# Optimization experiments

Hardware: AMD Instinct MI355X
Metric: run time of the kernel (lower is better)

## Reference

```python
import jax, jax.numpy as jnp
import numpy as np

NUM_HEADS = 4
DIM_MODEL = 256
DIM_HEAD = DIM_MODEL // NUM_HEADS  # 64


def _conv1x1(w, b, x):
    # Conv1d kernel_size=1: [B, D_in, N] -> [B, D_out, N]
    return jnp.einsum('oi,bin->bon', w, x) + b[None, :, None]


def setup_inputs() -> dict:
    key = jax.random.key(0)
    ks = jax.random.split(key, 12)
    B, D, N = 8, DIM_MODEL, 2048
    s = 1.0 / np.sqrt(D)
    inp = {
        'query': jax.random.normal(ks[0], (B, D, N), dtype=jnp.float32),
        'key': jax.random.normal(ks[1], (B, D, N), dtype=jnp.float32),
        'value': jax.random.normal(ks[2], (B, D, N), dtype=jnp.float32),
        'wq': jax.random.normal(ks[3], (D, D), dtype=jnp.float32) * s,
        'bq': jax.random.normal(ks[4], (D,), dtype=jnp.float32) * 0.01,
        'wk': jax.random.normal(ks[5], (D, D), dtype=jnp.float32) * s,
        'bk': jax.random.normal(ks[6], (D,), dtype=jnp.float32) * 0.01,
        'wv': jax.random.normal(ks[7], (D, D), dtype=jnp.float32) * s,
        'bv': jax.random.normal(ks[8], (D,), dtype=jnp.float32) * 0.01,
        'wm': jax.random.normal(ks[9], (D, D), dtype=jnp.float32) * s,
        'bm': jax.random.normal(ks[10], (D,), dtype=jnp.float32) * 0.01,
    }
    return inp


def reference(query, key, value, wq, bq, wk, bk, wv, bv, wm, bm):
    B = query.shape[0]
    d, h = DIM_HEAD, NUM_HEADS
    # 1x1 conv projections, then split channels as (dim_head, num_heads) per torch view
    q = _conv1x1(wq, bq, query).reshape(B, d, h, -1)  # [B, d, h, N]
    k = _conv1x1(wk, bk, key).reshape(B, d, h, -1)    # [B, d, h, M]
    v = _conv1x1(wv, bv, value).reshape(B, d, h, -1)  # [B, d, h, M]
    norm = 1.0 / float(d) ** 0.5
    scores = jnp.einsum('bdhn,bdhm->bhnm', q, k) * norm  # [B, h, N, M]
    prob = jax.nn.softmax(scores, axis=-1)
    attn = jnp.einsum('bhnm,bdhm->bdhn', prob, v)        # [B, d, h, N]
    out = _conv1x1(wm, bm, attn.reshape(B, d * h, -1))   # [B, D, N]
    return out
```

## Files before the change

kernel.cpp:

```cpp
#include <hip/hip_runtime.h>
#include <math.h>

#define BB 8
#define DD 256
#define NN 2048
#define NH 4
#define DH 64

typedef _Float16 half8   __attribute__((ext_vector_type(8)));
typedef _Float16 half4_t __attribute__((ext_vector_type(4)));
typedef float    floatx4 __attribute__((ext_vector_type(4)));

#define MFMA32(A, B, C) __builtin_amdgcn_mfma_f32_16x16x32_f16(A, B, C, 0, 0, 0)
#define MFMA16(A, B, C) __builtin_amdgcn_mfma_f32_16x16x16f16(A, B, C, 0, 0, 0)

#define SC 0.18033688011112042f

__global__ __launch_bounds__(256) void prep_weights(
    const float* __restrict__ wq, const float* __restrict__ wk,
    const float* __restrict__ wv, const float* __restrict__ wm,
    _Float16* __restrict__ wqf, _Float16* __restrict__ wkf,
    _Float16* __restrict__ wvf, _Float16* __restrict__ wmf)
{
    int id = blockIdx.x * 256 + threadIdx.x;
    wqf[id] = (_Float16)wq[id];
    wkf[id] = (_Float16)wk[id];
    wvf[id] = (_Float16)wv[id];
    int row = id >> 8, col = id & 255;
    int hh = col >> 6, dd = col & 63;
    wmf[id] = (_Float16)wm[row * 256 + dd * 4 + hh];
}


#define CONV_KLOOP(Wf)                                                        \
    half8 af[2][4][2];                                                        \
    {                                                                         \
        const _Float16* wp = (Wf) + (size_t)(w * 64 + c) * 256;               \
        _Pragma("unroll")                                                     \
        for (int rt = 0; rt < 4; ++rt)                                        \
            _Pragma("unroll")                                                 \
            for (int ch = 0; ch < 2; ++ch)                                    \
                af[0][rt][ch] =                                               \
                    *(const half8*)(wp + rt * 16 * 256 + ch * 32 + q * 8);    \
    }                                                                         \
    floatx4 acc[4][2];                                                        \
    _Pragma("unroll")                                                         \
    for (int rt = 0; rt < 4; ++rt)                                            \
        _Pragma("unroll")                                                     \
        for (int nt = 0; nt < 2; ++nt)                                        \
            acc[rt][nt] = (floatx4){0.f, 0.f, 0.f, 0.f};                      \
    _Pragma("unroll")                                                         \
    for (int kc = 0; kc < 4; ++kc) {                                          \
        const int cur = kc & 1;                                               \
        if (kc < 3) {                                                         \
            const _Float16* wp = (Wf) + (size_t)(w * 64 + c) * 256 +          \
                                 (kc + 1) * 64;                               \
            _Pragma("unroll")                                                 \
            for (int rt = 0; rt < 4; ++rt)                                    \
                _Pragma("unroll")                                             \
                for (int ch = 0; ch < 2; ++ch)                                \
                    af[cur ^ 1][rt][ch] = *(const half8*)(wp +                \
                        rt * 16 * 256 + ch * 32 + q * 8);                     \
        }                                                                     \
        half8 bx[2][2];                                                       \
        _Pragma("unroll")                                                     \
        for (int nt = 0; nt < 2; ++nt)                                        \
            _Pragma("unroll")                                                 \
            for (int ch = 0; ch < 2; ++ch)                                    \
                bx[nt][ch] = *(const half8*)(smem + (nt * 16 + c) * 264 +     \
                                             kc * 64 + ch * 32 + q * 8);      \
        _Pragma("unroll")                                                     \
        for (int nt = 0; nt < 2; ++nt)                                        \
            _Pragma("unroll")                                                 \
            for (int ch = 0; ch < 2; ++ch)                                    \
                _Pragma("unroll")                                             \
                for (int rt = 0; rt < 4; ++rt)                                \
                    acc[rt][nt] = MFMA32(af[cur][rt][ch], bx[nt][ch],         \
                                         acc[rt][nt]);                        \
    }

#define CONV_STAGE_F32(X)                                                     \
    {                                                                         \
        const int nb = t & 7, kb = t >> 3;                                    \
        const float* Xg = (X) + (size_t)b * DD * NN + (size_t)(kb * 8) * NN + \
                          n0 + nb * 4;                                        \
        float4 x[8];                                                          \
        _Pragma("unroll")                                                     \
        for (int i = 0; i < 8; ++i) x[i] = *(const float4*)(Xg + (size_t)i * NN); \
        _Pragma("unroll")                                                     \
        for (int j = 0; j < 4; ++j) {                                         \
            half8 hv;                                                         \
            _Pragma("unroll")                                                 \
            for (int i = 0; i < 8; ++i)                                       \
                hv[i] = (_Float16)(((const float*)&x[i])[j]);                 \
            *(half8*)(smem + (nb * 4 + j) * 264 + kb * 8) = hv;               \
        }                                                                     \
    }                                                                         \
    __syncthreads();

__global__ __launch_bounds__(256, 3) void conv_qk(
    const _Float16* __restrict__ wqf, const _Float16* __restrict__ wkf,
    const float* __restrict__ bq, const float* __restrict__ bk,
    const float* __restrict__ Xq, const float* __restrict__ Xk,
    _Float16* __restrict__ Yq, _Float16* __restrict__ Yk)
{
    const int n0 = blockIdx.x * 32;
    const int b  = blockIdx.y;
    const int pr = blockIdx.z;
    const _Float16* Wf = pr ? wkf : wqf;
    const float* bias  = pr ? bk : bq;
    const float* X     = pr ? Xk : Xq;
    _Float16* Y        = pr ? Yk : Yq;
    const float osc    = pr ? 1.0f : SC;

    const int t = threadIdx.x;
    const int w = t >> 6, l = t & 63, c = l & 15, q = l >> 4;

    __shared__ _Float16 smem[10240];

    CONV_STAGE_F32(X)
    CONV_KLOOP(Wf)

    __syncthreads();
    #pragma unroll
    for (int rt = 0; rt < 4; ++rt)
        #pragma unroll
        for (int nt = 0; nt < 2; ++nt) {
            half4_t hv;
            #pragma unroll
            for (int r = 0; r < 4; ++r)
                hv[r] = (_Float16)((acc[rt][nt][r] +
                        bias[w * 64 + rt * 16 + q * 4 + r]) * osc);
            *(half4_t*)(smem + (nt * 16 + c) * 264 + w * 64 + rt * 16 + q * 4) = hv;
        }
    __syncthreads();
    {
        const int rh = t >> 1, nn = rh >> 2, hh = rh & 3, off = (t & 1) * 32;
        const _Float16* src = smem + nn * 264 + hh;
        half8 hv[4];
        #pragma unroll
        for (int i = 0; i < 4; ++i)
            #pragma unroll
            for (int k = 0; k < 8; ++k)
                hv[i][k] = src[(off + i * 8 + k) * 4];
        _Float16* dst = Y + ((size_t)(b * NH + hh) * NN + n0 + nn) * 64 + off;
        #pragma unroll
        for (int i = 0; i < 4; ++i) *(half8*)(dst + i * 8) = hv[i];
    }
}

__global__ __launch_bounds__(256, 3) void conv_v(
    const _Float16* __restrict__ Wf, const float* __restrict__ bias,
    const float* __restrict__ X, _Float16* __restrict__ Y)
{
    const int n0 = blockIdx.x * 32;
    const int b  = blockIdx.y;
    const int t  = threadIdx.x;
    const int w  = t >> 6, l = t & 63, c = l & 15, q = l >> 4;

    __shared__ _Float16 smem[10240];

    CONV_STAGE_F32(X)
    CONV_KLOOP(Wf)

    __syncthreads();
    #pragma unroll
    for (int rt = 0; rt < 4; ++rt)
        #pragma unroll
        for (int nt = 0; nt < 2; ++nt)
            #pragma unroll
            for (int r = 0; r < 4; ++r)
                smem[(w * 64 + rt * 16 + q * 4 + r) * 40 + nt * 16 + c] =
                    (_Float16)(acc[rt][nt][r] + bias[w * 64 + rt * 16 + q * 4 + r]);
    __syncthreads();
    {
        const int dd = t >> 2, hh = t & 3;
        _Float16* dst = Y + ((size_t)(b * NH + hh) * 64 + dd) * NN + n0;
        #pragma unroll
        for (int i = 0; i < 4; ++i)
            *(half8*)(dst + i * 8) = *(const half8*)(smem + t * 40 + i * 8);
    }
}

__global__ __launch_bounds__(256, 3) void conv_o(
    const _Float16* __restrict__ Wf, const float* __restrict__ bias,
    const _Float16* __restrict__ At, float* __restrict__ out)
{
    const int n0 = blockIdx.x * 32;
    const int b  = blockIdx.y;
    const int t  = threadIdx.x;
    const int w  = t >> 6, l = t & 63, c = l & 15, q = l >> 4;

    __shared__ _Float16 smem[10240];

    {
        const int row = t >> 3, seg = (t & 7) * 32;
        const _Float16* Xg = At + ((size_t)b * NN + n0 + row) * 256 + seg;
        #pragma unroll
        for (int i = 0; i < 4; ++i)
            *(half8*)(smem + row * 264 + seg + i * 8) = *(const half8*)(Xg + i * 8);
    }
    __syncthreads();

    CONV_KLOOP(Wf)

    float* fs = (float*)smem;
    #pragma unroll
    for (int p = 0; p < 2; ++p) {
        __syncthreads();
        #pragma unroll
        for (int rtl = 0; rtl < 2; ++rtl) {
            const int rt = 2 * p + rtl;
            #pragma unroll
            for (int nt = 0; nt < 2; ++nt)
                #pragma unroll
                for (int r = 0; r < 4; ++r)
                    fs[(w * 32 + rtl * 16 + q * 4 + r) * 36 + nt * 16 + c] =
                        acc[rt][nt][r] + bias[w * 64 + rt * 16 + q * 4 + r];
        }
        __syncthreads();
        const int L = t >> 1, nloc = (t & 1) * 16;
        const int ww = L >> 5, rtl2 = (L >> 4) & 1, qq = (L >> 2) & 3, rr = L & 3;
        const int cout = ww * 64 + (2 * p + rtl2) * 16 + qq * 4 + rr;
        float* dst = out + (size_t)b * DD * NN + (size_t)cout * NN + n0 + nloc;
        #pragma unroll
        for (int i = 0; i < 4; ++i)
            *(float4*)(dst + 4 * i) = *(const float4*)(fs + L * 36 + nloc + 4 * i);
    }
}

__global__ __launch_bounds__(512) void attn_mfma4(
    const _Float16* __restrict__ Qt, const _Float16* __restrict__ Kt,
    const _Float16* __restrict__ V, _Float16* __restrict__ At)
{
    const int n0 = blockIdx.x * 128;
    const int h  = blockIdx.y;
    const int b  = blockIdx.z;
    const int t  = threadIdx.x;
    const int w  = t >> 6, l = t & 63, c = l & 15, q = l >> 4;

    const size_t bh = (size_t)(b * NH + h);

    __shared__ _Float16 smem[9216 + 8704];
    _Float16* Ks = smem;
    _Float16* Vs = smem + 9216;

    half8 bq2[2];
    #pragma unroll
    for (int ch = 0; ch < 2; ++ch)
        bq2[ch] = *(const half8*)(Qt + (bh * NN + n0 + w * 16 + c) * 64 + ch * 32 + q * 8);

    float lp = 0.f;
    floatx4 o[4];
    #pragma unroll
    for (int dt = 0; dt < 4; ++dt) o[dt] = (floatx4){0.f, 0.f, 0.f, 0.f};

    const int ksr = t >> 2, ksc = (t & 3) * 16;
    const int vr  = t >> 3, vcb = (t & 7) * 16;
    const _Float16* Kg = Kt + bh * NN * 64;
    const _Float16* Vg = V + bh * 64 * NN;

    for (int m0 = 0; m0 < NN; m0 += 128) {
        __syncthreads();
        *(half8*)(Ks + ksr * 72 + ksc) =
            *(const half8*)(Kg + (size_t)(m0 + ksr) * 64 + ksc);
        *(half8*)(Ks + ksr * 72 + ksc + 8) =
            *(const half8*)(Kg + (size_t)(m0 + ksr) * 64 + ksc + 8);
        #pragma unroll
        for (int u = 0; u < 2; ++u) {
            const int mb = vcb + u * 8;
            half8 v8 = *(const half8*)(Vg + (size_t)vr * NN + m0 + mb);
            const int p0 = (mb & ~31) + (((mb >> 2) & 3) << 3) + (((mb >> 4) & 1) << 2);
            half4_t lo, hi;
            #pragma unroll
            for (int j = 0; j < 4; ++j) { lo[j] = v8[j]; hi[j] = v8[4 + j]; }
            *(half4_t*)(Vs + vr * 136 + p0)     = lo;
            *(half4_t*)(Vs + vr * 136 + p0 + 8) = hi;
        }
        __syncthreads();

        #pragma unroll
        for (int mt2 = 0; mt2 < 4; ++mt2) {
            half4_t p[2];
            #pragma unroll
            for (int hf = 0; hf < 2; ++hf) {
                const int mt = mt2 * 2 + hf;
                floatx4 s = {0.f, 0.f, 0.f, 0.f};
                #pragma unroll
                for (int ch = 0; ch < 2; ++ch) {
                    half8 ak = *(const half8*)(Ks + (mt * 16 + c) * 72 + ch * 32 + q * 8);
                    s = MFMA32(ak, bq2[ch], s);
                }
                #pragma unroll
                for (int r = 0; r < 4; ++r) {
                    float e = exp2f(s[r]);
                    lp += e;
                    p[hf][r] = (_Float16)e;
                }
            }
            #pragma unroll
            for (int dt = 0; dt < 4; ++dt) {
                half8 av = *(const half8*)(Vs + (dt * 16 + c) * 136 + mt2 * 32 + q * 8);
                half4_t alo, ahi;
                #pragma unroll
                for (int j = 0; j < 4; ++j) { alo[j] = av[j]; ahi[j] = av[4 + j]; }
                o[dt] = MFMA16(alo, p[0], o[dt]);
                o[dt] = MFMA16(ahi, p[1], o[dt]);
            }
        }
    }

    lp += __shfl_xor(lp, 16);
    lp += __shfl_xor(lp, 32);
    const float inv = 1.f / lp;

    __syncthreads();
    #pragma unroll
    for (int dt = 0; dt < 4; ++dt) {
        half4_t ov;
        #pragma unroll
        for (int r = 0; r < 4; ++r) ov[r] = (_Float16)(o[dt][r] * inv);
        *(half4_t*)(smem + (w * 16 + c) * 72 + dt * 16 + q * 4) = ov;
    }
    __syncthreads();

    const int rn = t >> 2, roff = (t & 3) * 16;
    _Float16* dst = At + ((size_t)b * NN + n0 + rn) * 256 + h * 64 + roff;
    *(half8*)dst       = *(const half8*)(smem + rn * 72 + roff);
    *(half8*)(dst + 8) = *(const half8*)(smem + rn * 72 + roff + 8);
}

extern "C" void kernel_launch(void* const* d_in, const int* in_sizes, int n_in,
                              void* d_out, int out_size, void* d_ws, size_t ws_size,
                              hipStream_t stream) {
    const float* query = (const float*)d_in[0];
    const float* key_  = (const float*)d_in[1];
    const float* value = (const float*)d_in[2];
    const float* wq    = (const float*)d_in[3];
    const float* bq    = (const float*)d_in[4];
    const float* wk    = (const float*)d_in[5];
    const float* bk    = (const float*)d_in[6];
    const float* wv    = (const float*)d_in[7];
    const float* bv    = (const float*)d_in[8];
    const float* wm    = (const float*)d_in[9];
    const float* bm    = (const float*)d_in[10];
    float* out = (float*)d_out;

    _Float16* ws = (_Float16*)d_ws;
    _Float16* wqf = ws;
    _Float16* wkf = wqf + 65536;
    _Float16* wvf = wkf + 65536;
    _Float16* wmf = wvf + 65536;
    const size_t e16 = (size_t)BB * NH * NN * DH;
    _Float16* qf = ws + 262144;
    _Float16* kf = qf + e16;
    _Float16* vf = kf + e16;
    _Float16* at = vf + e16;

    prep_weights<<<256, 256, 0, stream>>>(wq, wk, wv, wm, wqf, wkf, wvf, wmf);
    conv_qk<<<dim3(64, 8, 2), 256, 0, stream>>>(wqf, wkf, bq, bk, query, key_, qf, kf);
    conv_v <<<dim3(64, 8, 1), 256, 0, stream>>>(wvf, bv, value, vf);
    attn_mfma4<<<dim3(16, 4, 8), 512, 0, stream>>>(qf, kf, vf, at);
    conv_o <<<dim3(64, 8, 1), 256, 0, stream>>>(wmf, bm, at, out);
}
```

Baseline: 218.0 us.

## Fuse Q/K/V projections into one launch, widen conv blocks, prefetch K/V in attention

Merges the separate Q/K and V projection kernels into a single conv_qkv launch with a z-dimension of three. The projection and output conv kernels move to 512-thread blocks that split the N tile across waves, each wave holding one accumulator column. The attention kernel gains register prefetching of the next K/V tile so the global loads overlap the MFMA work, and it uses packed cvt_pkrtz for the fp16 conversion of the exponentials. The aim is to cut launch overhead, shorten per-thread work and hide global-load latency, at the cost of more registers per thread in attention and round-toward-zero conversion instead of round-to-nearest.

```diff
diff --git a/kernel.cpp b/kernel.cpp
--- a/kernel.cpp
+++ b/kernel.cpp
@@ -9,6 +9,7 @@
 
 typedef _Float16 half8   __attribute__((ext_vector_type(8)));
 typedef _Float16 half4_t __attribute__((ext_vector_type(4)));
+typedef _Float16 half2_t __attribute__((ext_vector_type(2)));
 typedef float    floatx4 __attribute__((ext_vector_type(4)));
 
 #define MFMA32(A, B, C) __builtin_amdgcn_mfma_f32_16x16x32_f16(A, B, C, 0, 0, 0)
@@ -35,7 +36,7 @@
 #define CONV_KLOOP(Wf)                                                        \
     half8 af[2][4][2];                                                        \
     {                                                                         \
-        const _Float16* wp = (Wf) + (size_t)(w * 64 + c) * 256;               \
+        const _Float16* wp = (Wf) + (size_t)((w & 3) * 64 + c) * 256;         \
         _Pragma("unroll")                                                     \
         for (int rt = 0; rt < 4; ++rt)                                        \
             _Pragma("unroll")                                                 \
@@ -43,17 +44,14 @@
                 af[0][rt][ch] =                                               \
                     *(const half8*)(wp + rt * 16 * 256 + ch * 32 + q * 8);    \
     }                                                                         \
-    floatx4 acc[4][2];                                                        \
+    floatx4 acc[4];                                                           \
     _Pragma("unroll")                                                         \
-    for (int rt = 0; rt < 4; ++rt)                                            \
-        _Pragma("unroll")                                                     \
-        for (int nt = 0; nt < 2; ++nt)                                        \
-            acc[rt][nt] = (floatx4){0.f, 0.f, 0.f, 0.f};                      \
+    for (int rt = 0; rt < 4; ++rt) acc[rt] = (floatx4){0.f, 0.f, 0.f, 0.f};   \
     _Pragma("unroll")                                                         \
     for (int kc = 0; kc < 4; ++kc) {                                          \
         const int cur = kc & 1;                                               \
         if (kc < 3) {                                                         \
-            const _Float16* wp = (Wf) + (size_t)(w * 64 + c) * 256 +          \
+            const _Float16* wp = (Wf) + (size_t)((w & 3) * 64 + c) * 256 +    \
                                  (kc + 1) * 64;                               \
             _Pragma("unroll")                                                 \
             for (int rt = 0; rt < 4; ++rt)                                    \
@@ -62,127 +60,108 @@
                     af[cur ^ 1][rt][ch] = *(const half8*)(wp +                \
                         rt * 16 * 256 + ch * 32 + q * 8);                     \
         }                                                                     \
-        half8 bx[2][2];                                                       \
         _Pragma("unroll")                                                     \
-        for (int nt = 0; nt < 2; ++nt)                                        \
+        for (int ch = 0; ch < 2; ++ch) {                                      \
+            half8 bx = *(const half8*)(smem + ((w >> 2) * 16 + c) * 264 +     \
+                                       kc * 64 + ch * 32 + q * 8);            \
             _Pragma("unroll")                                                 \
-            for (int ch = 0; ch < 2; ++ch)                                    \
-                bx[nt][ch] = *(const half8*)(smem + (nt * 16 + c) * 264 +     \
-                                             kc * 64 + ch * 32 + q * 8);      \
-        _Pragma("unroll")                                                     \
-        for (int nt = 0; nt < 2; ++nt)                                        \
-            _Pragma("unroll")                                                 \
-            for (int ch = 0; ch < 2; ++ch)                                    \
-                _Pragma("unroll")                                             \
-                for (int rt = 0; rt < 4; ++rt)                                \
-                    acc[rt][nt] = MFMA32(af[cur][rt][ch], bx[nt][ch],         \
-                                         acc[rt][nt]);                        \
+            for (int rt = 0; rt < 4; ++rt)                                    \
+                acc[rt] = MFMA32(af[cur][rt][ch], bx, acc[rt]);               \
+        }                                                                     \
     }
 
 #define CONV_STAGE_F32(X)                                                     \
     {                                                                         \
         const int nb = t & 7, kb = t >> 3;                                    \
-        const float* Xg = (X) + (size_t)b * DD * NN + (size_t)(kb * 8) * NN + \
+        const float* Xg = (X) + (size_t)b * DD * NN + (size_t)(kb * 4) * NN + \
                           n0 + nb * 4;                                        \
-        float4 x[8];                                                          \
+        float4 x[4];                                                          \
         _Pragma("unroll")                                                     \
-        for (int i = 0; i < 8; ++i) x[i] = *(const float4*)(Xg + (size_t)i * NN); \
+        for (int i = 0; i < 4; ++i) x[i] = *(const float4*)(Xg + (size_t)i * NN); \
         _Pragma("unroll")                                                     \
         for (int j = 0; j < 4; ++j) {                                         \
-            half8 hv;                                                         \
+            half4_t hv;                                                       \
             _Pragma("unroll")                                                 \
-            for (int i = 0; i < 8; ++i)                                       \
+            for (int i = 0; i < 4; ++i)                                       \
                 hv[i] = (_Float16)(((const float*)&x[i])[j]);                 \
-            *(half8*)(smem + (nb * 4 + j) * 264 + kb * 8) = hv;               \
+            *(half4_t*)(smem + (nb * 4 + j) * 264 + kb * 4) = hv;             \
         }                                                                     \
     }                                                                         \
     __syncthreads();
 
-__global__ __launch_bounds__(256, 3) void conv_qk(
+__global__ __launch_bounds__(512, 4) void conv_qkv(
     const _Float16* __restrict__ wqf, const _Float16* __restrict__ wkf,
+    const _Float16* __restrict__ wvf,
     const float* __restrict__ bq, const float* __restrict__ bk,
+    const float* __restrict__ bv,
     const float* __restrict__ Xq, const float* __restrict__ Xk,
-    _Float16* __restrict__ Yq, _Float16* __restrict__ Yk)
+    const float* __restrict__ Xv,
+    _Float16* __restrict__ Yq, _Float16* __restrict__ Yk,
+    _Float16* __restrict__ Yv)
 {
     const int n0 = blockIdx.x * 32;
     const int b  = blockIdx.y;
-    const int pr = blockIdx.z;
-    const _Float16* Wf = pr ? wkf : wqf;
-    const float* bias  = pr ? bk : bq;
-    const float* X     = pr ? Xk : Xq;
-    _Float16* Y        = pr ? Yk : Yq;
-    const float osc    = pr ? 1.0f : SC;
+    const int z  = blockIdx.z;
+    const _Float16* Wf = z == 0 ? wqf : (z == 1 ? wkf : wvf);
+    const float* bias  = z == 0 ? bq  : (z == 1 ? bk  : bv);
+    const float* X     = z == 0 ? Xq  : (z == 1 ? Xk  : Xv);
+    const float osc    = z == 0 ? SC : 1.0f;
 
     const int t = threadIdx.x;
     const int w = t >> 6, l = t & 63, c = l & 15, q = l >> 4;
 
-    __shared__ _Float16 smem[10240];
+    __shared__ _Float16 smem[8704];
 
     CONV_STAGE_F32(X)
     CONV_KLOOP(Wf)
 
-    __syncthreads();
-    #pragma unroll
-    for (int rt = 0; rt < 4; ++rt)
-        #pragma unroll
-        for (int nt = 0; nt < 2; ++nt) {
+    if (z < 2) {
+        __syncthreads();
+        #pragma unroll
+        for (int rt = 0; rt < 4; ++rt) {
             half4_t hv;
             #pragma unroll
             for (int r = 0; r < 4; ++r)
-                hv[r] = (_Float16)((acc[rt][nt][r] +
-                        bias[w * 64 + rt * 16 + q * 4 + r]) * osc);
-            *(half4_t*)(smem + (nt * 16 + c) * 264 + w * 64 + rt * 16 + q * 4) = hv;
+                hv[r] = (_Float16)((acc[rt][r] +
+                        bias[(w & 3) * 64 + rt * 16 + q * 4 + r]) * osc);
+            *(half4_t*)(smem + ((w >> 2) * 16 + c) * 264 +
+                        (w & 3) * 64 + rt * 16 + q * 4) = hv;
         }
-    __syncthreads();
-    {
-        const int rh = t >> 1, nn = rh >> 2, hh = rh & 3, off = (t & 1) * 32;
+        __syncthreads();
+        _Float16* Y = z == 0 ? Yq : Yk;
+        const int pair = t >> 2;
+        const int nn = pair >> 2, hh = pair & 3;
+        const int doff = (t & 3) * 16;
         const _Float16* src = smem + nn * 264 + hh;
-        half8 hv[4];
-        #pragma unroll
-        for (int i = 0; i < 4; ++i)
+        half8 hv[2];
+        #pragma unroll
+        for (int i = 0; i < 2; ++i)
             #pragma unroll
             for (int k = 0; k < 8; ++k)
-                hv[i][k] = src[(off + i * 8 + k) * 4];
-        _Float16* dst = Y + ((size_t)(b * NH + hh) * NN + n0 + nn) * 64 + off;
-        #pragma unroll
-        for (int i = 0; i < 4; ++i) *(half8*)(dst + i * 8) = hv[i];
-    }
-}
-
-__global__ __launch_bounds__(256, 3) void conv_v(
-    const _Float16* __restrict__ Wf, const float* __restrict__ bias,
-    const float* __restrict__ X, _Float16* __restrict__ Y)
-{
-    const int n0 = blockIdx.x * 32;
-    const int b  = blockIdx.y;
-    const int t  = threadIdx.x;
-    const int w  = t >> 6, l = t & 63, c = l & 15, q = l >> 4;
-
-    __shared__ _Float16 smem[10240];
-
-    CONV_STAGE_F32(X)
-    CONV_KLOOP(Wf)
-
-    __syncthreads();
-    #pragma unroll
-    for (int rt = 0; rt < 4; ++rt)
-        #pragma unroll
-        for (int nt = 0; nt < 2; ++nt)
+                hv[i][k] = src[(doff + i * 8 + k) * 4];
+        _Float16* dst = Y + ((size_t)(b * NH + hh) * NN + n0 + nn) * 64 + doff;
+        *(half8*)dst       = hv[0];
+        *(half8*)(dst + 8) = hv[1];
+    } else {
+        __syncthreads();
+        #pragma unroll
+        for (int rt = 0; rt < 4; ++rt)
             #pragma unroll
             for (int r = 0; r < 4; ++r)
-                smem[(w * 64 + rt * 16 + q * 4 + r) * 40 + nt * 16 + c] =
-                    (_Float16)(acc[rt][nt][r] + bias[w * 64 + rt * 16 + q * 4 + r]);
-    __syncthreads();
-    {
-        const int dd = t >> 2, hh = t & 3;
-        _Float16* dst = Y + ((size_t)(b * NH + hh) * 64 + dd) * NN + n0;
-        #pragma unroll
-        for (int i = 0; i < 4; ++i)
-            *(half8*)(dst + i * 8) = *(const half8*)(smem + t * 40 + i * 8);
-    }
-}
-
-__global__ __launch_bounds__(256, 3) void conv_o(
+                smem[((w & 3) * 64 + rt * 16 + q * 4 + r) * 34 +
+                     (w >> 2) * 16 + c] =
+                    (_Float16)(acc[rt][r] +
+                               bias[(w & 3) * 64 + rt * 16 + q * 4 + r]);
+        __syncthreads();
+        const int cout = t >> 1, noff = (t & 1) * 16;
+        const int hh = cout & 3, dd = cout >> 2;
+        _Float16* dst = Yv + ((size_t)(b * NH + hh) * 64 + dd) * NN + n0 + noff;
+        *(half8*)dst       = *(const half8*)(smem + cout * 34 + noff);
+        *(half8*)(dst + 8) = *(const half8*)(smem + cout * 34 + noff + 8);
+    }
+}
+
+__global__ __launch_bounds__(512, 4) void conv_o(
     const _Float16* __restrict__ Wf, const float* __restrict__ bias,
     const _Float16* __restrict__ At, float* __restrict__ out)
 {
@@ -191,14 +170,13 @@
     const int t  = threadIdx.x;
     const int w  = t >> 6, l = t & 63, c = l & 15, q = l >> 4;
 
-    __shared__ _Float16 smem[10240];
+    __shared__ _Float16 smem[8704];
 
     {
-        const int row = t >> 3, seg = (t & 7) * 32;
+        const int row = t >> 4, seg = (t & 15) * 16;
         const _Float16* Xg = At + ((size_t)b * NN + n0 + row) * 256 + seg;
-        #pragma unroll
-        for (int i = 0; i < 4; ++i)
-            *(half8*)(smem + row * 264 + seg + i * 8) = *(const half8*)(Xg + i * 8);
+        *(half8*)(smem + row * 264 + seg)     = *(const half8*)(Xg);
+        *(half8*)(smem + row * 264 + seg + 8) = *(const half8*)(Xg + 8);
     }
     __syncthreads();
 
@@ -208,28 +186,25 @@
     #pragma unroll
     for (int p = 0; p < 2; ++p) {
         __syncthreads();
-        #pragma unroll
-        for (int rtl = 0; rtl < 2; ++rtl) {
-            const int rt = 2 * p + rtl;
-            #pragma unroll
-            for (int nt = 0; nt < 2; ++nt)
+        if (((w & 3) >> 1) == p) {
+            const int cl = ((w & 3) & 1) * 64;
+            #pragma unroll
+            for (int rt = 0; rt < 4; ++rt)
                 #pragma unroll
                 for (int r = 0; r < 4; ++r)
-                    fs[(w * 32 + rtl * 16 + q * 4 + r) * 36 + nt * 16 + c] =
-                        acc[rt][nt][r] + bias[w * 64 + rt * 16 + q * 4 + r];
+                    fs[(cl + rt * 16 + q * 4 + r) * 34 + (w >> 2) * 16 + c] =
+                        acc[rt][r] + bias[(w & 3) * 64 + rt * 16 + q * 4 + r];
         }
         __syncthreads();
-        const int L = t >> 1, nloc = (t & 1) * 16;
-        const int ww = L >> 5, rtl2 = (L >> 4) & 1, qq = (L >> 2) & 3, rr = L & 3;
-        const int cout = ww * 64 + (2 * p + rtl2) * 16 + qq * 4 + rr;
-        float* dst = out + (size_t)b * DD * NN + (size_t)cout * NN + n0 + nloc;
-        #pragma unroll
-        for (int i = 0; i < 4; ++i)
-            *(float4*)(dst + 4 * i) = *(const float4*)(fs + L * 36 + nloc + 4 * i);
-    }
-}
-
-__global__ __launch_bounds__(512) void attn_mfma4(
+        const int row = t >> 2, noff = (t & 3) * 8;
+        float* dst = out + (size_t)b * DD * NN +
+                     (size_t)(p * 128 + row) * NN + n0 + noff;
+        *(float4*)dst       = *(const float4*)(fs + row * 34 + noff);
+        *(float4*)(dst + 4) = *(const float4*)(fs + row * 34 + noff + 4);
+    }
+}
+
+__global__ __launch_bounds__(512) void attn_mfma5(
     const _Float16* __restrict__ Qt, const _Float16* __restrict__ Kt,
     const _Float16* __restrict__ V, _Float16* __restrict__ At)
 {
@@ -260,24 +235,33 @@
     const _Float16* Kg = Kt + bh * NN * 64;
     const _Float16* Vg = V + bh * 64 * NN;
 
+    half8 kpre[2], vpre[2];
+    kpre[0] = *(const half8*)(Kg + (size_t)ksr * 64 + ksc);
+    kpre[1] = *(const half8*)(Kg + (size_t)ksr * 64 + ksc + 8);
+    vpre[0] = *(const half8*)(Vg + (size_t)vr * NN + vcb);
+    vpre[1] = *(const half8*)(Vg + (size_t)vr * NN + vcb + 8);
+
     for (int m0 = 0; m0 < NN; m0 += 128) {
         __syncthreads();
-        *(half8*)(Ks + ksr * 72 + ksc) =
-            *(const half8*)(Kg + (size_t)(m0 + ksr) * 64 + ksc);
-        *(half8*)(Ks + ksr * 72 + ksc + 8) =
-            *(const half8*)(Kg + (size_t)(m0 + ksr) * 64 + ksc + 8);
+        *(half8*)(Ks + ksr * 72 + ksc)     = kpre[0];
+        *(half8*)(Ks + ksr * 72 + ksc + 8) = kpre[1];
         #pragma unroll
         for (int u = 0; u < 2; ++u) {
             const int mb = vcb + u * 8;
-            half8 v8 = *(const half8*)(Vg + (size_t)vr * NN + m0 + mb);
             const int p0 = (mb & ~31) + (((mb >> 2) & 3) << 3) + (((mb >> 4) & 1) << 2);
             half4_t lo, hi;
             #pragma unroll
-            for (int j = 0; j < 4; ++j) { lo[j] = v8[j]; hi[j] = v8[4 + j]; }
+            for (int j = 0; j < 4; ++j) { lo[j] = vpre[u][j]; hi[j] = vpre[u][4 + j]; }
             *(half4_t*)(Vs + vr * 136 + p0)     = lo;
             *(half4_t*)(Vs + vr * 136 + p0 + 8) = hi;
         }
         __syncthreads();
+
+        const int mn = (m0 + 128 < NN) ? m0 + 128 : m0;
+        kpre[0] = *(const half8*)(Kg + (size_t)(mn + ksr) * 64 + ksc);
+        kpre[1] = *(const half8*)(Kg + (size_t)(mn + ksr) * 64 + ksc + 8);
+        vpre[0] = *(const half8*)(Vg + (size_t)vr * NN + mn + vcb);
+        vpre[1] = *(const half8*)(Vg + (size_t)vr * NN + mn + vcb + 8);
 
         #pragma unroll
         for (int mt2 = 0; mt2 < 4; ++mt2) {
@@ -291,12 +275,13 @@
                     half8 ak = *(const half8*)(Ks + (mt * 16 + c) * 72 + ch * 32 + q * 8);
                     s = MFMA32(ak, bq2[ch], s);
                 }
-                #pragma unroll
-                for (int r = 0; r < 4; ++r) {
-                    float e = exp2f(s[r]);
-                    lp += e;
-                    p[hf][r] = (_Float16)e;
-                }
+                float e0 = exp2f(s[0]), e1 = exp2f(s[1]);
+                float e2 = exp2f(s[2]), e3 = exp2f(s[3]);
+                lp += (e0 + e1) + (e2 + e3);
+                half2_t c01 = __builtin_bit_cast(half2_t, __builtin_amdgcn_cvt_pkrtz(e0, e1));
+                half2_t c23 = __builtin_bit_cast(half2_t, __builtin_amdgcn_cvt_pkrtz(e2, e3));
+                p[hf][0] = c01[0]; p[hf][1] = c01[1];
+                p[hf][2] = c23[0]; p[hf][3] = c23[1];
             }
             #pragma unroll
             for (int dt = 0; dt < 4; ++dt) {
@@ -358,8 +343,8 @@
     _Float16* at = vf + e16;
 
     prep_weights<<<256, 256, 0, stream>>>(wq, wk, wv, wm, wqf, wkf, wvf, wmf);
-    conv_qk<<<dim3(64, 8, 2), 256, 0, stream>>>(wqf, wkf, bq, bk, query, key_, qf, kf);
-    conv_v <<<dim3(64, 8, 1), 256, 0, stream>>>(wvf, bv, value, vf);
-    attn_mfma4<<<dim3(16, 4, 8), 512, 0, stream>>>(qf, kf, vf, at);
-    conv_o <<<dim3(64, 8, 1), 256, 0, stream>>>(wmf, bm, at, out);
-}
+    conv_qkv<<<dim3(64, 8, 3), 512, 0, stream>>>(wqf, wkf, wvf, bq, bk, bv,
+                                                 query, key_, value, qf, kf, vf);
+    attn_mfma5<<<dim3(16, 4, 8), 512, 0, stream>>>(qf, kf, vf, at);
+    conv_o<<<dim3(64, 8), 512, 0, stream>>>(wmf, bm, at, out);
+}
```

Measured after the change: 227.9 us. 4.6% more time.
